# Kernel tuning notes

Hardware: AMD Instinct MI355X
Metric: run time of the kernel (lower is better)

## Reference

```python
import jax, jax.numpy as jnp
import numpy as np

B = 16384
N_NEIGH = 50
D = 64
NUM_USERS = 100000
NUM_ITEMS = 100000
NUM_ENTITIES = 200000


def setup_inputs() -> dict:
    key = jax.random.key(0)
    ks = jax.random.split(key, 16)
    s = 1.0 / np.sqrt(D)
    return {
        "user_indices": jax.random.randint(ks[0], (B,), 0, NUM_USERS),
        "item_indices": jax.random.randint(ks[1], (B,), 0, NUM_ITEMS),
        "kg_adj_batch": jax.random.randint(ks[2], (B, N_NEIGH), 0, NUM_ENTITIES),
        "user_table": jax.random.normal(ks[3], (NUM_USERS, D), jnp.float32),
        "item_table": jax.random.normal(ks[4], (NUM_ITEMS, D), jnp.float32),
        "entity_table": jax.random.normal(ks[5], (NUM_ENTITIES, D), jnp.float32),
        "attn_W": jax.random.normal(ks[6], (2 * D, 1), jnp.float32) * s,
        "attn_b": jnp.zeros((1,), jnp.float32),
        "kg_W1": jax.random.normal(ks[7], (D, D), jnp.float32) * s,
        "kg_b1": jnp.zeros((D,), jnp.float32),
        "kg_W2": jax.random.normal(ks[8], (D, D), jnp.float32) * s,
        "kg_b2": jnp.zeros((D,), jnp.float32),
        "comb_W": jax.random.normal(ks[9], (2 * D, D), jnp.float32) * s,
        "comb_b": jnp.zeros((D,), jnp.float32),
        "out_W": jax.random.normal(ks[10], (2 * D, 1), jnp.float32) * s,
        "out_b": jnp.zeros((1,), jnp.float32),
    }


def reference(user_indices, item_indices, kg_adj_batch,
              user_table, item_table, entity_table,
              attn_W, attn_b, kg_W1, kg_b1, kg_W2, kg_b2,
              comb_W, comb_b, out_W, out_b):
    user_emb = user_table[user_indices]          # [B, D]
    item_emb = item_table[item_indices]          # [B, D]
    nbr_idx = jnp.clip(kg_adj_batch, 0)
    neighbor_emb = entity_table[nbr_idx]         # [B, N, D]
    # attention_linear(cat([item, nbr])) == item @ Wi + nbr @ Wn + b (avoids [B,N,2D])
    Wi, Wn = attn_W[:D], attn_W[D:]
    attn_scores = item_emb @ Wi + jnp.einsum('bnd,do->bno', neighbor_emb, Wn)[..., 0] + attn_b  # [B, N]
    attn_scores = jax.nn.leaky_relu(attn_scores, negative_slope=0.2)
    attn_weights = jax.nn.softmax(attn_scores, axis=1)                 # softmax over neighbors
    neighbor_attn = jnp.einsum('bn,bnd->bd', attn_weights, neighbor_emb)
    refined_kg = jax.nn.relu(neighbor_attn @ kg_W1 + kg_b1) @ kg_W2 + kg_b2
    combined_item = jnp.concatenate([item_emb, refined_kg], axis=1)
    final_item_rep = jax.nn.relu(combined_item @ comb_W + comb_b)      # dropout = identity (eval)
    combined_user_item = jnp.concatenate([user_emb, final_item_rep], axis=1)
    score = (combined_user_item @ out_W + out_b)[:, 0]
    return score
```

## Files before the change

kernel.cpp:

```cpp
#include <hip/hip_runtime.h>

#define NN 50
#define D 64
#define GRP 10

typedef unsigned int uint32;
typedef unsigned short ushort16;

__device__ __forceinline__ float wave_sum64(float x) {
#pragma unroll
  for (int off = 32; off > 0; off >>= 1)
    x += __shfl_xor(x, off, 64);
  return x;
}

__device__ __forceinline__ float readlane_f(float v, int l) {
  return __uint_as_float(__builtin_amdgcn_readlane(__float_as_uint(v), l));
}

__device__ __forceinline__ ushort16 f32_to_bf16(float f) {
  uint32 u = __float_as_uint(f);
  u += 0x7FFF + ((u >> 16) & 1);
  return (ushort16)(u >> 16);
}
__device__ __forceinline__ float bf16_to_f32(ushort16 h) {
  return __uint_as_float(((uint32)h) << 16);
}

__global__ __launch_bounds__(256, 4) void ent_proj(
    const float* __restrict__ ent_tab, const float* __restrict__ attn_W,
    float* __restrict__ proj, ushort16* __restrict__ ent_bf, int rows)
{
  const int  lane = threadIdx.x & 63;
  const long wave = (long)blockIdx.x * 4 + (threadIdx.x >> 6);
  const long base = wave * GRP;
  if (base >= rows) return;
  const float Wn = attn_W[D + lane];
  float v[GRP];
#pragma unroll
  for (int i = 0; i < GRP; ++i) {
    long r = base + i; if (r > rows - 1) r = rows - 1;
    v[i] = ent_tab[r * D + lane];
  }
  float s[GRP];
#pragma unroll
  for (int i = 0; i < GRP; ++i)
    s[i] = wave_sum64(v[i] * Wn);
#pragma unroll
  for (int i = 0; i < GRP; ++i) {
    const long r = base + i;
    if (r < rows) ent_bf[r * D + lane] = f32_to_bf16(v[i]);
  }
  if (lane == 0) {
#pragma unroll
    for (int i = 0; i < GRP; ++i)
      if (base + i < rows) proj[base + i] = s[i];
  }
}

__device__ __forceinline__ void load_grp_bf(float (&buf)[GRP],
                                            const int* __restrict__ adjb,
                                            const ushort16* __restrict__ ent_bf,
                                            int g, int lane) {
#pragma unroll
  for (int i = 0; i < GRP; ++i) {
    int t = adjb[g * GRP + i];
    t = t < 0 ? 0 : t;
    buf[i] = bf16_to_f32(ent_bf[(long)t * D + lane]);
  }
}

__device__ __forceinline__ void acc_grp(const float (&buf)[GRP], float e, int g,
                                        float& na0, float& na1) {
#pragma unroll
  for (int i = 0; i < GRP; ++i) {
    const float w = readlane_f(e, g * GRP + i);
    if (i & 1) na1 = fmaf(w, buf[i], na1);
    else       na0 = fmaf(w, buf[i], na0);
  }
}

__device__ __forceinline__ void attn_elem(
    int b, const int* __restrict__ adj,
    const ushort16* __restrict__ ent_bf, const float* __restrict__ proj,
    const int* __restrict__ user_idx, const int* __restrict__ item_idx,
    const float* __restrict__ user_tab, const float* __restrict__ item_tab,
    const float* __restrict__ attn_W, float ab, int lane,
    float& na_out, float& item_out, float& user_out)
{
  const int* adjb = adj + (long)b * NN;

  const int myn = lane < NN ? lane : NN - 1;
  int mi = adjb[myn]; mi = mi < 0 ? 0 : mi;
  const float pj = proj[mi];
  user_out = user_tab[(long)user_idx[b] * D + lane];
  const float item = item_tab[(long)item_idx[b] * D + lane];

  float G0[GRP], G1[GRP], G2[GRP], G3[GRP], G4[GRP];
  load_grp_bf(G0, adjb, ent_bf, 0, lane);
  load_grp_bf(G1, adjb, ent_bf, 1, lane);
  load_grp_bf(G2, adjb, ent_bf, 2, lane);
  load_grp_bf(G3, adjb, ent_bf, 3, lane);
  load_grp_bf(G4, adjb, ent_bf, 4, lane);

  const float base = wave_sum64(item * attn_W[lane]) + ab;
  float s = pj + base;
  s = s > 0.f ? s : 0.2f * s;
  const float e = (lane < NN) ? __expf(s - 8.0f) : 0.f;
  const float denom = wave_sum64(e);

  float na0 = 0.f, na1 = 0.f;
  acc_grp(G0, e, 0, na0, na1);
  acc_grp(G1, e, 1, na0, na1);
  acc_grp(G2, e, 2, na0, na1);
  acc_grp(G3, e, 3, na0, na1);
  acc_grp(G4, e, 4, na0, na1);
  na_out = (na0 + na1) / denom;
  item_out = item;
}

__global__ __launch_bounds__(256, 2) void kgat_fused(
    const int* __restrict__ user_idx, const int* __restrict__ item_idx,
    const int* __restrict__ adj,
    const float* __restrict__ user_tab, const float* __restrict__ item_tab,
    const ushort16* __restrict__ ent_bf, const float* __restrict__ proj,
    const float* __restrict__ attn_W, const float* __restrict__ attn_b,
    const float* __restrict__ W1, const float* __restrict__ b1,
    const float* __restrict__ W2, const float* __restrict__ b2,
    const float* __restrict__ cW, const float* __restrict__ cb,
    const float* __restrict__ oW, const float* __restrict__ ob,
    float* __restrict__ out, int B)
{
  __shared__ __align__(16) float s_a0[4 * D], s_a1[4 * D];
  __shared__ __align__(16) float s_i0[4 * D], s_i1[4 * D];

  const int lane = threadIdx.x & 63;
  const int wv   = threadIdx.x >> 6;
  const int bA   = (blockIdx.x * 4 + wv) * 2;
  if (bA >= B) return;
  const int bB   = bA + 1 < B ? bA + 1 : bA;
  float* sa0 = s_a0 + wv * D;
  float* sa1 = s_a1 + wv * D;
  float* si0 = s_i0 + wv * D;
  float* si1 = s_i1 + wv * D;

  const float ab = attn_b[0];

  float naA, itA, usA, naB, itB, usB;
  attn_elem(bA, adj, ent_bf, proj, user_idx, item_idx,
            user_tab, item_tab, attn_W, ab, lane, naA, itA, usA);
  attn_elem(bB, adj, ent_bf, proj, user_idx, item_idx,
            user_tab, item_tab, attn_W, ab, lane, naB, itB, usB);

  sa0[lane] = naA; sa1[lane] = naB;
  si0[lane] = itA; si1[lane] = itB;

  const float b1v = b1[lane];
  float hA0 = b1v, hA1 = 0.f, hA2 = 0.f, hA3 = 0.f;
  float hB0 = b1v, hB1 = 0.f, hB2 = 0.f, hB3 = 0.f;
#pragma unroll
  for (int d = 0; d < D; d += 4) {
    const float4 cA = *(const float4*)(sa0 + d);
    const float4 cB = *(const float4*)(sa1 + d);
    const float w0 = W1[(d + 0) * D + lane];
    const float w1 = W1[(d + 1) * D + lane];
    const float w2 = W1[(d + 2) * D + lane];
    const float w3 = W1[(d + 3) * D + lane];
    hA0 = fmaf(cA.x, w0, hA0); hB0 = fmaf(cB.x, w0, hB0);
    hA1 = fmaf(cA.y, w1, hA1); hB1 = fmaf(cB.y, w1, hB1);
    hA2 = fmaf(cA.z, w2, hA2); hB2 = fmaf(cB.z, w2, hB2);
    hA3 = fmaf(cA.w, w3, hA3); hB3 = fmaf(cB.w, w3, hB3);
  }
  const float hA = fmaxf((hA0 + hA1) + (hA2 + hA3), 0.f);
  const float hB = fmaxf((hB0 + hB1) + (hB2 + hB3), 0.f);

  sa0[lane] = hA; sa1[lane] = hB;
  const float b2v = b2[lane];
  float rA0 = b2v, rA1 = 0.f, rA2 = 0.f, rA3 = 0.f;
  float rB0 = b2v, rB1 = 0.f, rB2 = 0.f, rB3 = 0.f;
#pragma unroll
  for (int d = 0; d < D; d += 4) {
    const float4 cA = *(const float4*)(sa0 + d);
    const float4 cB = *(const float4*)(sa1 + d);
    const float w0 = W2[(d + 0) * D + lane];
    const float w1 = W2[(d + 1) * D + lane];
    const float w2 = W2[(d + 2) * D + lane];
    const float w3 = W2[(d + 3) * D + lane];
    rA0 = fmaf(cA.x, w0, rA0); rB0 = fmaf(cB.x, w0, rB0);
    rA1 = fmaf(cA.y, w1, rA1); rB1 = fmaf(cB.y, w1, rB1);
    rA2 = fmaf(cA.z, w2, rA2); rB2 = fmaf(cB.z, w2, rB2);
    rA3 = fmaf(cA.w, w3, rA3); rB3 = fmaf(cB.w, w3, rB3);
  }
  const float rA = (rA0 + rA1) + (rA2 + rA3);
  const float rB = (rB0 + rB1) + (rB2 + rB3);

  sa0[lane] = rA; sa1[lane] = rB;
  const float cbv = cb[lane];
  float fA0 = cbv, fA1 = 0.f, fA2 = 0.f, fA3 = 0.f;
  float fB0 = cbv, fB1 = 0.f, fB2 = 0.f, fB3 = 0.f;
#pragma unroll
  for (int k = 0; k < D; k += 4) {
    const float4 cA = *(const float4*)(si0 + k);
    const float4 cB = *(const float4*)(si1 + k);
    const float w0 = cW[(k + 0) * D + lane];
    const float w1 = cW[(k + 1) * D + lane];
    const float w2 = cW[(k + 2) * D + lane];
    const float w3 = cW[(k + 3) * D + lane];
    fA0 = fmaf(cA.x, w0, fA0); fB0 = fmaf(cB.x, w0, fB0);
    fA1 = fmaf(cA.y, w1, fA1); fB1 = fmaf(cB.y, w1, fB1);
    fA2 = fmaf(cA.z, w2, fA2); fB2 = fmaf(cB.z, w2, fB2);
    fA3 = fmaf(cA.w, w3, fA3); fB3 = fmaf(cB.w, w3, fB3);
  }
#pragma unroll
  for (int k = 0; k < D; k += 4) {
    const float4 cA = *(const float4*)(sa0 + k);
    const float4 cB = *(const float4*)(sa1 + k);
    const float w0 = cW[(D + k + 0) * D + lane];
    const float w1 = cW[(D + k + 1) * D + lane];
    const float w2 = cW[(D + k + 2) * D + lane];
    const float w3 = cW[(D + k + 3) * D + lane];
    fA0 = fmaf(cA.x, w0, fA0); fB0 = fmaf(cB.x, w0, fB0);
    fA1 = fmaf(cA.y, w1, fA1); fB1 = fmaf(cB.y, w1, fB1);
    fA2 = fmaf(cA.z, w2, fA2); fB2 = fmaf(cB.z, w2, fB2);
    fA3 = fmaf(cA.w, w3, fA3); fB3 = fmaf(cB.w, w3, fB3);
  }
  const float fA = fmaxf((fA0 + fA1) + (fA2 + fA3), 0.f);
  const float fB = fmaxf((fB0 + fB1) + (fB2 + fB3), 0.f);

  const float oWu = oW[lane];
  const float oWf = oW[D + lane];
  const float ob0 = ob[0];
  const float scA = wave_sum64(fmaf(usA, oWu, fA * oWf));
  const float scB = wave_sum64(fmaf(usB, oWu, fB * oWf));
  if (lane == 0) {
    out[bA] = scA + ob0;
    if (bB != bA) out[bB] = scB + ob0;
  }
}

__device__ __forceinline__ void load_grp(float (&buf)[GRP],
                                         const int* __restrict__ adjb,
                                         const float* __restrict__ ent_tab,
                                         int g, int lane) {
#pragma unroll
  for (int i = 0; i < GRP; ++i) {
    int t = adjb[g * GRP + i];
    t = t < 0 ? 0 : t;
    buf[i] = ent_tab[(long)t * D + lane];
  }
}

__device__ __forceinline__ void proc_grp(const float (&buf)[GRP],
                                         float Wn, float base,
                                         float& l0, float& l1, float& na) {
  float ex[GRP];
#pragma unroll
  for (int i = 0; i < GRP; ++i) {
    float t = wave_sum64(buf[i] * Wn) + base;
    t = t > 0.f ? t : 0.2f * t;
    ex[i] = __expf(t - 8.0f);
  }
#pragma unroll
  for (int i = 0; i < GRP; ++i) {
    if (i & 1) l1 += ex[i]; else l0 += ex[i];
    na = fmaf(ex[i], buf[i], na);
  }
}

__global__ __launch_bounds__(256, 4) void kgat_r3(
    const int* __restrict__ user_idx, const int* __restrict__ item_idx,
    const int* __restrict__ adj,
    const float* __restrict__ user_tab, const float* __restrict__ item_tab,
    const float* __restrict__ ent_tab,
    const float* __restrict__ attn_W, const float* __restrict__ attn_b,
    const float* __restrict__ W1, const float* __restrict__ b1,
    const float* __restrict__ W2, const float* __restrict__ b2,
    const float* __restrict__ cW, const float* __restrict__ cb,
    const float* __restrict__ oW, const float* __restrict__ ob,
    float* __restrict__ out, int B)
{
  const int lane = threadIdx.x & 63;
  const int wv   = threadIdx.x >> 6;
  const int b    = blockIdx.x * 4 + wv;
  if (b >= B) return;

  const float user = user_tab[(long)user_idx[b] * D + lane];
  const float oWu  = oW[lane];
  const float oWf  = oW[D + lane];
  const float item = item_tab[(long)item_idx[b] * D + lane];
  const float Wi   = attn_W[lane];
  const float Wn   = attn_W[D + lane];
  const float base = wave_sum64(item * Wi) + attn_b[0];
  const int* adjb = adj + b * NN;

  float na = 0.f, l0 = 0.f, l1 = 0.f;
  float A[GRP], Bv[GRP];
  load_grp(A,  adjb, ent_tab, 0, lane);
  load_grp(Bv, adjb, ent_tab, 1, lane);
  proc_grp(A,  Wn, base, l0, l1, na);
  load_grp(A,  adjb, ent_tab, 2, lane);
  proc_grp(Bv, Wn, base, l0, l1, na);
  load_grp(Bv, adjb, ent_tab, 3, lane);
  proc_grp(A,  Wn, base, l0, l1, na);
  load_grp(A,  adjb, ent_tab, 4, lane);
  proc_grp(Bv, Wn, base, l0, l1, na);
  proc_grp(A,  Wn, base, l0, l1, na);
  na /= (l0 + l1);

  float h0 = b1[lane], h1 = 0.f, h2 = 0.f, h3 = 0.f;
#pragma unroll
  for (int d = 0; d < D; d += 4) {
    h0 = fmaf(readlane_f(na, d + 0), W1[(d + 0) * D + lane], h0);
    h1 = fmaf(readlane_f(na, d + 1), W1[(d + 1) * D + lane], h1);
    h2 = fmaf(readlane_f(na, d + 2), W1[(d + 2) * D + lane], h2);
    h3 = fmaf(readlane_f(na, d + 3), W1[(d + 3) * D + lane], h3);
  }
  const float h = fmaxf((h0 + h1) + (h2 + h3), 0.f);

  float r0 = b2[lane], r1 = 0.f, r2 = 0.f, r3 = 0.f;
#pragma unroll
  for (int d = 0; d < D; d += 4) {
    r0 = fmaf(readlane_f(h, d + 0), W2[(d + 0) * D + lane], r0);
    r1 = fmaf(readlane_f(h, d + 1), W2[(d + 1) * D + lane], r1);
    r2 = fmaf(readlane_f(h, d + 2), W2[(d + 2) * D + lane], r2);
    r3 = fmaf(readlane_f(h, d + 3), W2[(d + 3) * D + lane], r3);
  }
  const float r = (r0 + r1) + (r2 + r3);

  float f0 = cb[lane], f1 = 0.f, f2 = 0.f, f3 = 0.f;
#pragma unroll
  for (int k = 0; k < D; k += 4) {
    f0 = fmaf(readlane_f(item, k + 0), cW[(k + 0) * D + lane], f0);
    f1 = fmaf(readlane_f(item, k + 1), cW[(k + 1) * D + lane], f1);
    f2 = fmaf(readlane_f(item, k + 2), cW[(k + 2) * D + lane], f2);
    f3 = fmaf(readlane_f(item, k + 3), cW[(k + 3) * D + lane], f3);
  }
#pragma unroll
  for (int k = 0; k < D; k += 4) {
    f0 = fmaf(readlane_f(r, k + 0), cW[(D + k + 0) * D + lane], f0);
    f1 = fmaf(readlane_f(r, k + 1), cW[(D + k + 1) * D + lane], f1);
    f2 = fmaf(readlane_f(r, k + 2), cW[(D + k + 2) * D + lane], f2);
    f3 = fmaf(readlane_f(r, k + 3), cW[(D + k + 3) * D + lane], f3);
  }
  const float f = fmaxf((f0 + f1) + (f2 + f3), 0.f);

  const float sc = wave_sum64(fmaf(user, oWu, f * oWf));
  if (lane == 0) out[b] = sc + ob[0];
}

extern "C" void kernel_launch(void* const* d_in, const int* in_sizes, int n_in,
                              void* d_out, int out_size, void* d_ws, size_t ws_size,
                              hipStream_t stream) {
  const int*   user_idx = (const int*)d_in[0];
  const int*   item_idx = (const int*)d_in[1];
  const int*   adj      = (const int*)d_in[2];
  const float* user_tab = (const float*)d_in[3];
  const float* item_tab = (const float*)d_in[4];
  const float* ent_tab  = (const float*)d_in[5];
  const float* attn_W   = (const float*)d_in[6];
  const float* attn_b   = (const float*)d_in[7];
  const float* W1       = (const float*)d_in[8];
  const float* b1       = (const float*)d_in[9];
  const float* W2       = (const float*)d_in[10];
  const float* b2       = (const float*)d_in[11];
  const float* cW       = (const float*)d_in[12];
  const float* cb       = (const float*)d_in[13];
  const float* oW       = (const float*)d_in[14];
  const float* ob       = (const float*)d_in[15];
  float* out = (float*)d_out;

  const int B    = in_sizes[0];
  const int rows = in_sizes[5] / D;

  const size_t off_bf = ((size_t)rows * 4 + 255) & ~(size_t)255;
  const size_t need   = off_bf + (size_t)rows * D * 2;

  if (ws_size >= need) {
    float*    proj   = (float*)d_ws;
    ushort16* ent_bf = (ushort16*)((char*)d_ws + off_bf);
    const int waves   = (rows + GRP - 1) / GRP;
    const int pblocks = (waves + 3) / 4;
    const int fblocks = (B + 8 - 1) / 8;
    ent_proj<<<pblocks, 256, 0, stream>>>(ent_tab, attn_W, proj, ent_bf, rows);
    kgat_fused<<<fblocks, 256, 0, stream>>>(user_idx, item_idx, adj,
                                            user_tab, item_tab, ent_bf, proj,
                                            attn_W, attn_b, W1, b1, W2, b2,
                                            cW, cb, oW, ob, out, B);
  } else {
    const int blocks = (B + 3) / 4;
    kgat_r3<<<blocks, 256, 0, stream>>>(user_idx, item_idx, adj,
                                        user_tab, item_tab, ent_tab,
                                        attn_W, attn_b, W1, b1, W2, b2,
                                        cW, cb, oW, ob, out, B);
  }
}
```

Before: 58.74 us.

## Split attention gather and MLP into separate kernels with double-buffered neighbor loads

Splits the fused kernel into an attention kernel, one wave per batch row, that writes neighbor-attention vectors to a workspace buffer, and a separate MLP kernel that reads them back. The attention kernel holds two register buffers and interleaves loads with accumulation instead of holding all 50 rows at once, so it needs fewer registers and can run at higher occupancy (launch bounds 4). The cost is an extra kernel launch, a B×D float round trip through global memory, and re-reading the item embeddings in the MLP kernel.

```diff
diff --git a/kernel.cpp b/kernel.cpp
--- a/kernel.cpp
+++ b/kernel.cpp
@@ -80,51 +80,51 @@
   }
 }
 
-__device__ __forceinline__ void attn_elem(
-    int b, const int* __restrict__ adj,
+__global__ __launch_bounds__(256, 4) void kgat_attn(
+    const int* __restrict__ item_idx, const int* __restrict__ adj,
+    const float* __restrict__ item_tab,
     const ushort16* __restrict__ ent_bf, const float* __restrict__ proj,
-    const int* __restrict__ user_idx, const int* __restrict__ item_idx,
-    const float* __restrict__ user_tab, const float* __restrict__ item_tab,
-    const float* __restrict__ attn_W, float ab, int lane,
-    float& na_out, float& item_out, float& user_out)
+    const float* __restrict__ attn_W, const float* __restrict__ attn_b,
+    float* __restrict__ naws, int B)
 {
+  const int lane = threadIdx.x & 63;
+  const int wv   = threadIdx.x >> 6;
+  const int b    = blockIdx.x * 4 + wv;
+  if (b >= B) return;
+
   const int* adjb = adj + (long)b * NN;
+
+  float A[GRP], Bv[GRP];
+  load_grp_bf(A,  adjb, ent_bf, 0, lane);
+  load_grp_bf(Bv, adjb, ent_bf, 1, lane);
+
+  const float item = item_tab[(long)item_idx[b] * D + lane];
+  const float base = wave_sum64(item * attn_W[lane]) + attn_b[0];
 
   const int myn = lane < NN ? lane : NN - 1;
   int mi = adjb[myn]; mi = mi < 0 ? 0 : mi;
-  const float pj = proj[mi];
-  user_out = user_tab[(long)user_idx[b] * D + lane];
-  const float item = item_tab[(long)item_idx[b] * D + lane];
-
-  float G0[GRP], G1[GRP], G2[GRP], G3[GRP], G4[GRP];
-  load_grp_bf(G0, adjb, ent_bf, 0, lane);
-  load_grp_bf(G1, adjb, ent_bf, 1, lane);
-  load_grp_bf(G2, adjb, ent_bf, 2, lane);
-  load_grp_bf(G3, adjb, ent_bf, 3, lane);
-  load_grp_bf(G4, adjb, ent_bf, 4, lane);
-
-  const float base = wave_sum64(item * attn_W[lane]) + ab;
-  float s = pj + base;
+  float s = proj[mi] + base;
   s = s > 0.f ? s : 0.2f * s;
   const float e = (lane < NN) ? __expf(s - 8.0f) : 0.f;
   const float denom = wave_sum64(e);
 
   float na0 = 0.f, na1 = 0.f;
-  acc_grp(G0, e, 0, na0, na1);
-  acc_grp(G1, e, 1, na0, na1);
-  acc_grp(G2, e, 2, na0, na1);
-  acc_grp(G3, e, 3, na0, na1);
-  acc_grp(G4, e, 4, na0, na1);
-  na_out = (na0 + na1) / denom;
-  item_out = item;
-}
-
-__global__ __launch_bounds__(256, 2) void kgat_fused(
+  acc_grp(A,  e, 0, na0, na1);
+  load_grp_bf(A,  adjb, ent_bf, 2, lane);
+  acc_grp(Bv, e, 1, na0, na1);
+  load_grp_bf(Bv, adjb, ent_bf, 3, lane);
+  acc_grp(A,  e, 2, na0, na1);
+  load_grp_bf(A,  adjb, ent_bf, 4, lane);
+  acc_grp(Bv, e, 3, na0, na1);
+  acc_grp(A,  e, 4, na0, na1);
+
+  naws[(long)b * D + lane] = (na0 + na1) / denom;
+}
+
+__global__ __launch_bounds__(256, 4) void kgat_mlp2(
     const int* __restrict__ user_idx, const int* __restrict__ item_idx,
-    const int* __restrict__ adj,
     const float* __restrict__ user_tab, const float* __restrict__ item_tab,
-    const ushort16* __restrict__ ent_bf, const float* __restrict__ proj,
-    const float* __restrict__ attn_W, const float* __restrict__ attn_b,
+    const float* __restrict__ naws,
     const float* __restrict__ W1, const float* __restrict__ b1,
     const float* __restrict__ W2, const float* __restrict__ b2,
     const float* __restrict__ cW, const float* __restrict__ cb,
@@ -144,13 +144,12 @@
   float* si0 = s_i0 + wv * D;
   float* si1 = s_i1 + wv * D;
 
-  const float ab = attn_b[0];
-
-  float naA, itA, usA, naB, itB, usB;
-  attn_elem(bA, adj, ent_bf, proj, user_idx, item_idx,
-            user_tab, item_tab, attn_W, ab, lane, naA, itA, usA);
-  attn_elem(bB, adj, ent_bf, proj, user_idx, item_idx,
-            user_tab, item_tab, attn_W, ab, lane, naB, itB, usB);
+  const float naA = naws[(long)bA * D + lane];
+  const float naB = naws[(long)bB * D + lane];
+  const float itA = item_tab[(long)item_idx[bA] * D + lane];
+  const float itB = item_tab[(long)item_idx[bB] * D + lane];
+  const float usA = user_tab[(long)user_idx[bA] * D + lane];
+  const float usB = user_tab[(long)user_idx[bB] * D + lane];
 
   sa0[lane] = naA; sa1[lane] = naB;
   si0[lane] = itA; si1[lane] = itB;
@@ -373,19 +372,23 @@
   const int rows = in_sizes[5] / D;
 
   const size_t off_bf = ((size_t)rows * 4 + 255) & ~(size_t)255;
-  const size_t need   = off_bf + (size_t)rows * D * 2;
+  const size_t off_na = (off_bf + (size_t)rows * D * 2 + 255) & ~(size_t)255;
+  const size_t need   = off_na + (size_t)B * D * 4;
 
   if (ws_size >= need) {
     float*    proj   = (float*)d_ws;
     ushort16* ent_bf = (ushort16*)((char*)d_ws + off_bf);
+    float*    naws   = (float*)((char*)d_ws + off_na);
     const int waves   = (rows + GRP - 1) / GRP;
     const int pblocks = (waves + 3) / 4;
-    const int fblocks = (B + 8 - 1) / 8;
+    const int ablocks = (B + 3) / 4;
+    const int mblocks = (B + 7) / 8;
     ent_proj<<<pblocks, 256, 0, stream>>>(ent_tab, attn_W, proj, ent_bf, rows);
-    kgat_fused<<<fblocks, 256, 0, stream>>>(user_idx, item_idx, adj,
-                                            user_tab, item_tab, ent_bf, proj,
-                                            attn_W, attn_b, W1, b1, W2, b2,
-                                            cW, cb, oW, ob, out, B);
+    kgat_attn<<<ablocks, 256, 0, stream>>>(item_idx, adj, item_tab, ent_bf,
+                                           proj, attn_W, attn_b, naws, B);
+    kgat_mlp2<<<mblocks, 256, 0, stream>>>(user_idx, item_idx, user_tab,
+                                           item_tab, naws, W1, b1, W2, b2,
+                                           cW, cb, oW, ob, out, B);
   } else {
     const int blocks = (B + 3) / 4;
     kgat_r3<<<blocks, 256, 0, stream>>>(user_idx, item_idx, adj,
```

After: 62.31 us. 1.06x slower.
